# Kernel optimization log

Hardware: AMD Instinct MI355X
Metric: run time of the kernel (lower is better)

## Reference

```python
import jax, jax.numpy as jnp
import numpy as np

N, D, H, O, E = 8192, 512, 2048, 512, 8

def setup_inputs() -> dict:
    key = jax.random.key(0)
    ks = jax.random.split(key, 7)
    s = lambda *sh: 1.0 / np.sqrt(sh[-2] if len(sh) > 1 else 1.0)
    x  = jax.random.normal(ks[0], (N, D), dtype=jnp.float32)
    Wr = jax.random.normal(ks[1], (D, E), dtype=jnp.float32) * (1.0 / np.sqrt(D))
    br = jnp.zeros((E,), dtype=jnp.float32)
    W1 = jax.random.normal(ks[2], (E, D, H), dtype=jnp.float32) * (1.0 / np.sqrt(D))
    b1 = jnp.zeros((E, H), dtype=jnp.float32)
    W2 = jax.random.normal(ks[3], (E, H, O), dtype=jnp.float32) * (1.0 / np.sqrt(H))
    b2 = jnp.zeros((E, O), dtype=jnp.float32)
    return {"x": x, "Wr": Wr, "br": br, "W1": W1, "b1": b1, "W2": W2, "b2": b2}


def reference(x, Wr, br, W1, b1, W2, b2):
    # --- supervised router step: Linear -> softmax -> max ---
    router_logits = x @ Wr + br                      # [N, E]
    router_probs = jax.nn.softmax(router_logits, axis=-1)
    p_max = jnp.max(router_probs, axis=-1)           # [N]
    routes = jnp.argmax(router_probs, axis=-1)       # [N] int
    onehot = jax.nn.one_hot(routes, W1.shape[0], dtype=x.dtype)  # [N, E] dispatch mask

    # --- per-expert MLP (dense reference for the gather/compute/scatter pattern) ---
    h = jax.nn.relu(jnp.einsum('nd,edh->enh', x, W1) + b1[:, None, :])  # [E, N, H]
    all_out = jnp.einsum('enh,eho->eno', h, W2) + b2[:, None, :]        # [E, N, O]

    # --- combine: each token takes its routed expert's output ---
    out = jnp.einsum('ne,eno->no', onehot, all_out)  # [N, O]

    # straight-through scaling: value 1 in fwd, routes gradient into router probs
    scale = p_max / jax.lax.stop_gradient(p_max)
    logits = out * scale[:, None]

    counts = jnp.sum(onehot, axis=0)                 # tokens per expert
    return logits, router_probs, counts
```

## Files before the change

kernel.cpp:

```cpp
#include <hip/hip_runtime.h>
#include <hip/hip_bf16.h>
#include <stdint.h>

#define N_TOK 8192
#define DIM   512
#define HID   2048
#define OUTD  512
#define NEXP  8

typedef short  bf16x8 __attribute__((ext_vector_type(8)));
typedef float  f32x4  __attribute__((ext_vector_type(4)));
typedef unsigned short u16x8 __attribute__((ext_vector_type(8)));
typedef unsigned short u16x4 __attribute__((ext_vector_type(4)));

#define WS_CNT    0
#define WS_LIST   4096
#define WS_XBF    266240
#define WS_W1T    8654848
#define WS_W2T    25432064
#define WS_H      42209280

__device__ __forceinline__ unsigned short f2bf(float f) {
    uint32_t u = __builtin_bit_cast(uint32_t, f);
    u = (u + 0x7fffu + ((u >> 16) & 1u)) >> 16;
    return (unsigned short)u;
}

__device__ __forceinline__ void gload16(const unsigned short* g, unsigned short* l) {
    __builtin_amdgcn_global_load_lds(
        (const __attribute__((address_space(1))) unsigned int*)g,
        (__attribute__((address_space(3))) unsigned int*)l, 16, 0, 0);
}

#define MFMA_BF16 __builtin_amdgcn_mfma_f32_16x16x32_bf16

__global__ __launch_bounds__(256) void prep_kernel(
    const float* __restrict__ x, const float* __restrict__ wr, const float* __restrict__ br,
    const float* __restrict__ w1, const float* __restrict__ w2,
    float* __restrict__ probs, int* __restrict__ cnt, int* __restrict__ list,
    unsigned short* __restrict__ xbf, unsigned short* __restrict__ w1t, unsigned short* __restrict__ w2t)
{
    const int bid = blockIdx.x, tid = threadIdx.x;
    if (bid < 32) {
        __shared__ int lcnt[NEXP];
        __shared__ int lbase[NEXP];
        if (tid < NEXP) lcnt[tid] = 0;
        __syncthreads();
        const int n = bid * 256 + tid;
        float acc[NEXP];
        #pragma unroll
        for (int e = 0; e < NEXP; e++) acc[e] = br[e];
        const f32x4* xr = (const f32x4*)(x + (size_t)n * DIM);
        for (int i = 0; i < DIM / 4; i++) {
            f32x4 v = xr[i];
            #pragma unroll
            for (int d = 0; d < 4; d++) {
                const float xv = v[d];
                #pragma unroll
                for (int e = 0; e < NEXP; e++)
                    acc[e] += xv * wr[(i * 4 + d) * NEXP + e];
            }
        }
        float mx = acc[0]; int am = 0;
        #pragma unroll
        for (int e = 1; e < NEXP; e++) if (acc[e] > mx) { mx = acc[e]; am = e; }
        float p[NEXP]; float s = 0.f;
        #pragma unroll
        for (int e = 0; e < NEXP; e++) { p[e] = expf(acc[e] - mx); s += p[e]; }
        const float inv = 1.f / s;
        f32x4 p0, p1;
        #pragma unroll
        for (int e = 0; e < 4; e++) { p0[e] = p[e] * inv; p1[e] = p[e + 4] * inv; }
        *(f32x4*)&probs[(size_t)n * NEXP]     = p0;
        *(f32x4*)&probs[(size_t)n * NEXP + 4] = p1;
        const int slot = atomicAdd(&lcnt[am], 1);
        __syncthreads();
        if (tid < NEXP) lbase[tid] = atomicAdd(&cnt[tid], lcnt[tid]);
        __syncthreads();
        list[am * N_TOK + lbase[am] + slot] = n;
    } else if (bid < 2080) {
        const size_t i = (size_t)(bid - 32) * 256 + tid;
        f32x4 a = *(const f32x4*)&x[i * 8];
        f32x4 b = *(const f32x4*)&x[i * 8 + 4];
        u16x8 o;
        #pragma unroll
        for (int j = 0; j < 4; j++) { o[j] = f2bf(a[j]); o[4 + j] = f2bf(b[j]); }
        *(u16x8*)&xbf[i * 8] = o;
    } else {
        __shared__ float t[32][33];
        const float* pin; unsigned short* pout; int R, C, r0, c0;
        if (bid < 10272) {
            const int loc = bid - 2080, e = loc >> 10, l2 = loc & 1023;
            pin = w1 + (size_t)e * DIM * HID; pout = w1t + (size_t)e * DIM * HID;
            R = DIM; C = HID; r0 = (l2 >> 6) * 32; c0 = (l2 & 63) * 32;
        } else {
            const int loc = bid - 10272, e = loc >> 10, l2 = loc & 1023;
            pin = w2 + (size_t)e * HID * OUTD; pout = w2t + (size_t)e * HID * OUTD;
            R = HID; C = OUTD; r0 = (l2 >> 4) * 32; c0 = (l2 & 15) * 32;
        }
        const int lr = tid >> 3, lc4 = (tid & 7) * 4;
        f32x4 v = *(const f32x4*)&pin[(size_t)(r0 + lr) * C + c0 + lc4];
        #pragma unroll
        for (int i = 0; i < 4; i++) t[lr][lc4 + i] = v[i];
        __syncthreads();
        u16x4 o;
        #pragma unroll
        for (int i = 0; i < 4; i++) o[i] = f2bf(t[lc4 + i][lr]);
        *(u16x4*)&pout[(size_t)(c0 + lr) * R + r0 + lc4] = o;
    }
}

__device__ __forceinline__ int xcd_swizzle(int bid, int nwg, bool& valid) {
    const int xcd = bid & 7, cidx = bid >> 3;
    const int q = nwg >> 3, r = nwg & 7;
    const int csz = q + (xcd < r ? 1 : 0);
    valid = (cidx < csz);
    return (xcd < r ? xcd * (q + 1) : r * (q + 1) + (xcd - r) * q) + cidx;
}

template<int SH>
__device__ __forceinline__ void tile_map(const int* __restrict__ cnt, int tile,
                                         int& e, int& row0, int& bs, int& m_e, int& ntiles) {
    const int G = 1 << SH, GM = G - 1;
    int c[NEXP]; ntiles = 0;
    #pragma unroll
    for (int i = 0; i < NEXP; i++) { c[i] = cnt[i]; ntiles += (c[i] + GM) >> SH; }
    int t = tile, b = 0, ei = 0;
    #pragma unroll
    for (int i = 0; i < NEXP; i++) {
        const int nt = (c[i] + GM) >> SH;
        if (t >= 0 && t < nt) { ei = i; row0 = t << SH; bs = b; m_e = c[i]; }
        t -= nt; b += c[i];
    }
    e = ei;
}

__global__ __launch_bounds__(512, 4) void gemm1_kernel(
    const unsigned short* __restrict__ xbf, const unsigned short* __restrict__ w1t,
    const float* __restrict__ b1, const int* __restrict__ list,
    const int* __restrict__ cnt, unsigned short* __restrict__ h)
{
    int e = 0, row0 = 0, bs = 0, m_e = 0, ntm = 0;
    tile_map<7>(cnt, 0, e, row0, bs, m_e, ntm);
    const int nwg = ntm * 8;
    bool valid; const int v = xcd_swizzle(blockIdx.x, nwg, valid);
    if (!valid) return;
    const int tile = v >> 3, ntile = v & 7;
    tile_map<7>(cnt, tile, e, row0, bs, m_e, ntm);
    const int n0 = ntile * 256;

    __shared__ unsigned short ldsA[128 * 64] __attribute__((aligned(16)));
    __shared__ unsigned short ldsB[256 * 64] __attribute__((aligned(16)));
    __shared__ int ldsTok[128];
    const int tid = threadIdx.x;
    if (tid < 128) { int r = row0 + tid; if (r >= m_e) r = m_e - 1; ldsTok[tid] = list[e * N_TOK + r]; }
    __syncthreads();

    const int gslot = tid & 7;
    const unsigned short* aSrc[2]; const unsigned short* bSrc[4];
    #pragma unroll
    for (int g = 0; g < 2; g++) {
        const int row = (g * 512 + tid) >> 3;
        const int col = ((gslot ^ (row & 7)) << 3);
        aSrc[g] = xbf + (size_t)ldsTok[row] * DIM + col;
    }
    #pragma unroll
    for (int g = 0; g < 4; g++) {
        const int row = (g * 512 + tid) >> 3;
        const int col = ((gslot ^ (row & 7)) << 3);
        bSrc[g] = w1t + ((size_t)e * HID + n0 + row) * DIM + col;
    }

    f32x4 acc[4][4] = {};
    const int lane = tid & 63, wid = tid >> 6;
    const int wr = wid >> 2, wc = wid & 3;
    const int lrow = lane & 15, gk = lane >> 4, lm = lrow & 7;

    int rowA[4], rowB[4];
    #pragma unroll
    for (int f = 0; f < 4; f++) rowA[f] = (wr * 64 + f * 16 + lrow) * 64;
    #pragma unroll
    for (int f = 0; f < 4; f++) rowB[f] = (wc * 64 + f * 16 + lrow) * 64;

    for (int t = 0; t < 8; t++) {
        const int k0 = t * 64;
        __syncthreads();
        #pragma unroll
        for (int g = 0; g < 2; g++)
            gload16(aSrc[g] + k0, ldsA + ((g << 9) + (tid & 448)) * 8);
        #pragma unroll
        for (int g = 0; g < 4; g++)
            gload16(bSrc[g] + k0, ldsB + ((g << 9) + (tid & 448)) * 8);
        __syncthreads();
        #pragma unroll
        for (int kk = 0; kk < 2; kk++) {
            bf16x8 av[4], bv[4];
            #pragma unroll
            for (int f = 0; f < 4; f++)
                av[f] = *(const bf16x8*)&ldsA[rowA[f] + ((((kk << 2) + gk) ^ lm) << 3)];
            #pragma unroll
            for (int f = 0; f < 4; f++)
                bv[f] = *(const bf16x8*)&ldsB[rowB[f] + ((((kk << 2) + gk) ^ lm) << 3)];
            #pragma unroll
            for (int mf = 0; mf < 4; mf++)
                #pragma unroll
                for (int nf = 0; nf < 4; nf++)
                    acc[mf][nf] = MFMA_BF16(av[mf], bv[nf], acc[mf][nf], 0, 0, 0);
        }
    }

    const int hbase = bs + row0;
    float bias[4];
    #pragma unroll
    for (int nf = 0; nf < 4; nf++) bias[nf] = b1[e * HID + n0 + wc * 64 + nf * 16 + lrow];
    #pragma unroll
    for (int mf = 0; mf < 4; mf++) {
        #pragma unroll
        for (int j = 0; j < 4; j++) {
            const int m = wr * 64 + mf * 16 + gk * 4 + j;
            if (row0 + m < m_e) {
                const size_t ro = (size_t)(hbase + m) * HID + n0 + wc * 64;
                #pragma unroll
                for (int nf = 0; nf < 4; nf++) {
                    float vv = acc[mf][nf][j] + bias[nf];
                    h[ro + nf * 16 + lrow] = f2bf(vv > 0.f ? vv : 0.f);
                }
            }
        }
    }
}

__global__ __launch_bounds__(256) void gemm2_kernel(
    const unsigned short* __restrict__ h, const unsigned short* __restrict__ w2t,
    const float* __restrict__ b2, const int* __restrict__ list,
    const int* __restrict__ cnt, float* __restrict__ out, float* __restrict__ counts)
{
    const int tid = threadIdx.x;
    if (blockIdx.x == 0 && tid < NEXP) counts[tid] = (float)cnt[tid];

    int e = 0, row0 = 0, bs = 0, m_e = 0, ntm = 0;
    tile_map<7>(cnt, 0, e, row0, bs, m_e, ntm);
    const int nwg = ntm * 8;
    bool valid; const int v = xcd_swizzle(blockIdx.x, nwg, valid);
    if (!valid) return;
    const int tile = v >> 3, ntile = v & 7;
    tile_map<7>(cnt, tile, e, row0, bs, m_e, ntm);
    const int n0 = ntile * 64;

    __shared__ unsigned short ldsA[128 * 64] __attribute__((aligned(16)));
    __shared__ unsigned short ldsB[64 * 64]  __attribute__((aligned(16)));
    __shared__ int ldsTok[128];
    if (tid < 128) { int r = row0 + tid; if (r >= m_e) r = m_e - 1; ldsTok[tid] = list[e * N_TOK + r]; }
    __syncthreads();

    const int gslot = tid & 7;
    const unsigned short* aSrc[4]; const unsigned short* bSrc[2];
    #pragma unroll
    for (int i = 0; i < 4; i++) {
        const int row = (i * 256 + tid) >> 3;
        const int col = ((gslot ^ (row & 7)) << 3);
        int slot = row0 + row; if (slot >= m_e) slot = m_e - 1;
        aSrc[i] = h + (size_t)(bs + slot) * HID + col;
    }
    #pragma unroll
    for (int i = 0; i < 2; i++) {
        const int row = (i * 256 + tid) >> 3;
        const int col = ((gslot ^ (row & 7)) << 3);
        bSrc[i] = w2t + ((size_t)e * OUTD + n0 + row) * HID + col;
    }

    f32x4 acc[4][2] = {};
    const int lane = tid & 63, wid = tid >> 6;
    const int wm = (wid >> 1) * 64, wn = (wid & 1) * 32;
    const int lrow = lane & 15, gk = lane >> 4, lm = lrow & 7;

    int rowA[4], rowB[2];
    #pragma unroll
    for (int f = 0; f < 4; f++) rowA[f] = (wm + f * 16 + lrow) * 64;
    #pragma unroll
    for (int f = 0; f < 2; f++) rowB[f] = (wn + f * 16 + lrow) * 64;

    for (int t = 0; t < 32; t++) {
        const int k0 = t * 64;
        __syncthreads();
        #pragma unroll
        for (int i = 0; i < 4; i++)
            gload16(aSrc[i] + k0, ldsA + ((i << 8) + (tid & 192)) * 8);
        #pragma unroll
        for (int i = 0; i < 2; i++)
            gload16(bSrc[i] + k0, ldsB + ((i << 8) + (tid & 192)) * 8);
        __syncthreads();
        #pragma unroll
        for (int kk = 0; kk < 2; kk++) {
            bf16x8 av[4], bv[2];
            #pragma unroll
            for (int f = 0; f < 4; f++)
                av[f] = *(const bf16x8*)&ldsA[rowA[f] + ((((kk << 2) + gk) ^ lm) << 3)];
            #pragma unroll
            for (int f = 0; f < 2; f++)
                bv[f] = *(const bf16x8*)&ldsB[rowB[f] + ((((kk << 2) + gk) ^ lm) << 3)];
            #pragma unroll
            for (int mf = 0; mf < 4; mf++)
                #pragma unroll
                for (int nf = 0; nf < 2; nf++)
                    acc[mf][nf] = MFMA_BF16(av[mf], bv[nf], acc[mf][nf], 0, 0, 0);
        }
    }

    float bias[2];
    #pragma unroll
    for (int nf = 0; nf < 2; nf++) bias[nf] = b2[e * OUTD + n0 + wn + nf * 16 + lrow];
    #pragma unroll
    for (int mf = 0; mf < 4; mf++) {
        #pragma unroll
        for (int j = 0; j < 4; j++) {
            const int m = wm + mf * 16 + gk * 4 + j;
            if (row0 + m < m_e) {
                const size_t ro = (size_t)ldsTok[m] * OUTD + n0 + wn;
                #pragma unroll
                for (int nf = 0; nf < 2; nf++)
                    out[ro + nf * 16 + lrow] = acc[mf][nf][j] + bias[nf];
            }
        }
    }
}

extern "C" void kernel_launch(void* const* d_in, const int* in_sizes, int n_in,
                              void* d_out, int out_size, void* d_ws, size_t ws_size,
                              hipStream_t stream) {
    (void)in_sizes; (void)n_in; (void)out_size; (void)ws_size;
    const float* x  = (const float*)d_in[0];
    const float* wr = (const float*)d_in[1];
    const float* br = (const float*)d_in[2];
    const float* w1 = (const float*)d_in[3];
    const float* b1 = (const float*)d_in[4];
    const float* w2 = (const float*)d_in[5];
    const float* b2 = (const float*)d_in[6];

    float* out    = (float*)d_out;
    float* probs  = out + (size_t)N_TOK * OUTD;
    float* counts = probs + (size_t)N_TOK * NEXP;

    char* ws = (char*)d_ws;
    int* cnt     = (int*)(ws + WS_CNT);
    int* list    = (int*)(ws + WS_LIST);
    unsigned short* xbf = (unsigned short*)(ws + WS_XBF);
    unsigned short* w1t = (unsigned short*)(ws + WS_W1T);
    unsigned short* w2t = (unsigned short*)(ws + WS_W2T);
    unsigned short* hbf = (unsigned short*)(ws + WS_H);

    hipMemsetAsync(cnt, 0, NEXP * sizeof(int), stream);
    prep_kernel<<<18464, 256, 0, stream>>>(x, wr, br, w1, w2, probs, cnt, list, xbf, w1t, w2t);
    gemm1_kernel<<<576, 512, 0, stream>>>(xbf, w1t, b1, list, cnt, hbf);
    gemm2_kernel<<<576, 256, 0, stream>>>(hbf, w2t, b2, list, cnt, out, counts);
}
```

Measured before the change: 112.2 us.

## Split router into own kernel and enlarge weight transpose tiles to 64x64

Moves the router/softmax/dispatch work out of the combined prep kernel into a separate 32-block launch. The weight transpose-and-convert now uses 64x64 tiles with 16-element-per-thread loads and 16-byte bf16 stores instead of 32x32 tiles with 8-byte stores, cutting the block count and widening writes. The aim is less per-block overhead and better store coalescing in the memory-bound prep phase. The cost is an extra kernel launch, plus the router no longer overlapping with the conversion blocks.

```diff
diff --git a/kernel.cpp b/kernel.cpp
--- a/kernel.cpp
+++ b/kernel.cpp
@@ -34,79 +34,93 @@
 
 #define MFMA_BF16 __builtin_amdgcn_mfma_f32_16x16x32_bf16
 
-__global__ __launch_bounds__(256) void prep_kernel(
-    const float* __restrict__ x, const float* __restrict__ wr, const float* __restrict__ br,
-    const float* __restrict__ w1, const float* __restrict__ w2,
-    float* __restrict__ probs, int* __restrict__ cnt, int* __restrict__ list,
-    unsigned short* __restrict__ xbf, unsigned short* __restrict__ w1t, unsigned short* __restrict__ w2t)
+__global__ __launch_bounds__(256) void router_kernel(
+    const float* __restrict__ x, const float* __restrict__ wr,
+    const float* __restrict__ br, float* __restrict__ probs,
+    int* __restrict__ cnt, int* __restrict__ list)
+{
+    __shared__ int lcnt[NEXP];
+    __shared__ int lbase[NEXP];
+    const int tid = threadIdx.x;
+    if (tid < NEXP) lcnt[tid] = 0;
+    __syncthreads();
+
+    const int n = blockIdx.x * 256 + tid;
+    float acc[NEXP];
+    #pragma unroll
+    for (int e = 0; e < NEXP; e++) acc[e] = br[e];
+
+    const f32x4* xr = (const f32x4*)(x + (size_t)n * DIM);
+    for (int i = 0; i < DIM / 4; i++) {
+        f32x4 v = xr[i];
+        #pragma unroll
+        for (int d = 0; d < 4; d++) {
+            const float xv = v[d];
+            #pragma unroll
+            for (int e = 0; e < NEXP; e++)
+                acc[e] += xv * wr[(i * 4 + d) * NEXP + e];
+        }
+    }
+    float mx = acc[0]; int am = 0;
+    #pragma unroll
+    for (int e = 1; e < NEXP; e++) if (acc[e] > mx) { mx = acc[e]; am = e; }
+    float p[NEXP]; float s = 0.f;
+    #pragma unroll
+    for (int e = 0; e < NEXP; e++) { p[e] = expf(acc[e] - mx); s += p[e]; }
+    const float inv = 1.f / s;
+    f32x4 p0, p1;
+    #pragma unroll
+    for (int e = 0; e < 4; e++) { p0[e] = p[e] * inv; p1[e] = p[e + 4] * inv; }
+    *(f32x4*)&probs[(size_t)n * NEXP]     = p0;
+    *(f32x4*)&probs[(size_t)n * NEXP + 4] = p1;
+
+    const int slot = atomicAdd(&lcnt[am], 1);
+    __syncthreads();
+    if (tid < NEXP) lbase[tid] = atomicAdd(&cnt[tid], lcnt[tid]);
+    __syncthreads();
+    list[am * N_TOK + lbase[am] + slot] = n;
+}
+
+__global__ __launch_bounds__(256) void stream_prep_kernel(
+    const float* __restrict__ x, const float* __restrict__ w1, const float* __restrict__ w2,
+    unsigned short* __restrict__ xbf, unsigned short* __restrict__ w1t,
+    unsigned short* __restrict__ w2t)
 {
     const int bid = blockIdx.x, tid = threadIdx.x;
-    if (bid < 32) {
-        __shared__ int lcnt[NEXP];
-        __shared__ int lbase[NEXP];
-        if (tid < NEXP) lcnt[tid] = 0;
-        __syncthreads();
-        const int n = bid * 256 + tid;
-        float acc[NEXP];
-        #pragma unroll
-        for (int e = 0; e < NEXP; e++) acc[e] = br[e];
-        const f32x4* xr = (const f32x4*)(x + (size_t)n * DIM);
-        for (int i = 0; i < DIM / 4; i++) {
-            f32x4 v = xr[i];
-            #pragma unroll
-            for (int d = 0; d < 4; d++) {
-                const float xv = v[d];
-                #pragma unroll
-                for (int e = 0; e < NEXP; e++)
-                    acc[e] += xv * wr[(i * 4 + d) * NEXP + e];
-            }
-        }
-        float mx = acc[0]; int am = 0;
-        #pragma unroll
-        for (int e = 1; e < NEXP; e++) if (acc[e] > mx) { mx = acc[e]; am = e; }
-        float p[NEXP]; float s = 0.f;
-        #pragma unroll
-        for (int e = 0; e < NEXP; e++) { p[e] = expf(acc[e] - mx); s += p[e]; }
-        const float inv = 1.f / s;
-        f32x4 p0, p1;
-        #pragma unroll
-        for (int e = 0; e < 4; e++) { p0[e] = p[e] * inv; p1[e] = p[e + 4] * inv; }
-        *(f32x4*)&probs[(size_t)n * NEXP]     = p0;
-        *(f32x4*)&probs[(size_t)n * NEXP + 4] = p1;
-        const int slot = atomicAdd(&lcnt[am], 1);
-        __syncthreads();
-        if (tid < NEXP) lbase[tid] = atomicAdd(&cnt[tid], lcnt[tid]);
-        __syncthreads();
-        list[am * N_TOK + lbase[am] + slot] = n;
-    } else if (bid < 2080) {
-        const size_t i = (size_t)(bid - 32) * 256 + tid;
+    if (bid < 4096) {
+        __shared__ float t[64][65];
+        const float* pin; unsigned short* pout; int R, C, r0, c0;
+        if (bid < 2048) {
+            const int e = bid >> 8, l2 = bid & 255;
+            pin = w1 + (size_t)e * DIM * HID; pout = w1t + (size_t)e * DIM * HID;
+            R = DIM; C = HID; r0 = (l2 >> 5) * 64; c0 = (l2 & 31) * 64;
+        } else {
+            const int loc = bid - 2048, e = loc >> 8, l2 = loc & 255;
+            pin = w2 + (size_t)e * HID * OUTD; pout = w2t + (size_t)e * HID * OUTD;
+            R = HID; C = OUTD; r0 = (l2 >> 3) * 64; c0 = (l2 & 7) * 64;
+        }
+        const int r = tid >> 2, q = tid & 3;
+        #pragma unroll
+        for (int j = 0; j < 4; j++) {
+            f32x4 v = *(const f32x4*)&pin[(size_t)(r0 + r) * C + c0 + q * 16 + j * 4];
+            #pragma unroll
+            for (int i = 0; i < 4; i++) t[r][q * 16 + j * 4 + i] = v[i];
+        }
+        __syncthreads();
+        unsigned short o[16];
+        #pragma unroll
+        for (int i = 0; i < 16; i++) o[i] = f2bf(t[q * 16 + i][r]);
+        unsigned short* dst = &pout[(size_t)(c0 + r) * R + r0 + q * 16];
+        *(u16x8*)dst       = *(const u16x8*)&o[0];
+        *(u16x8*)(dst + 8) = *(const u16x8*)&o[8];
+    } else {
+        const size_t i = (size_t)(bid - 4096) * 256 + tid;
         f32x4 a = *(const f32x4*)&x[i * 8];
         f32x4 b = *(const f32x4*)&x[i * 8 + 4];
         u16x8 o;
         #pragma unroll
         for (int j = 0; j < 4; j++) { o[j] = f2bf(a[j]); o[4 + j] = f2bf(b[j]); }
         *(u16x8*)&xbf[i * 8] = o;
-    } else {
-        __shared__ float t[32][33];
-        const float* pin; unsigned short* pout; int R, C, r0, c0;
-        if (bid < 10272) {
-            const int loc = bid - 2080, e = loc >> 10, l2 = loc & 1023;
-            pin = w1 + (size_t)e * DIM * HID; pout = w1t + (size_t)e * DIM * HID;
-            R = DIM; C = HID; r0 = (l2 >> 6) * 32; c0 = (l2 & 63) * 32;
-        } else {
-            const int loc = bid - 10272, e = loc >> 10, l2 = loc & 1023;
-            pin = w2 + (size_t)e * HID * OUTD; pout = w2t + (size_t)e * HID * OUTD;
-            R = HID; C = OUTD; r0 = (l2 >> 4) * 32; c0 = (l2 & 15) * 32;
-        }
-        const int lr = tid >> 3, lc4 = (tid & 7) * 4;
-        f32x4 v = *(const f32x4*)&pin[(size_t)(r0 + lr) * C + c0 + lc4];
-        #pragma unroll
-        for (int i = 0; i < 4; i++) t[lr][lc4 + i] = v[i];
-        __syncthreads();
-        u16x4 o;
-        #pragma unroll
-        for (int i = 0; i < 4; i++) o[i] = f2bf(t[lc4 + i][lr]);
-        *(u16x4*)&pout[(size_t)(c0 + lr) * R + r0 + lc4] = o;
     }
 }
 
@@ -350,7 +364,8 @@
     unsigned short* hbf = (unsigned short*)(ws + WS_H);
 
     hipMemsetAsync(cnt, 0, NEXP * sizeof(int), stream);
-    prep_kernel<<<18464, 256, 0, stream>>>(x, wr, br, w1, w2, probs, cnt, list, xbf, w1t, w2t);
+    router_kernel<<<32, 256, 0, stream>>>(x, wr, br, probs, cnt, list);
+    stream_prep_kernel<<<6144, 256, 0, stream>>>(x, w1, w2, xbf, w1t, w2t);
     gemm1_kernel<<<576, 512, 0, stream>>>(xbf, w1t, b1, list, cnt, hbf);
     gemm2_kernel<<<576, 256, 0, stream>>>(hbf, w2t, b2, list, cnt, out, counts);
 }
```

Measured after the change: 121.7 us. +8.5%, slower.
